# Performance work log

Measured on AMD Instinct MI355X. Metric: run time of the kernel, lower is better.

The kernel has to match this reference:

```python
import jax, jax.numpy as jnp
import numpy as np

B, L, D = 16, 2048, 256

def setup_inputs() -> dict:
    key = jax.random.key(0)
    k1, k2 = jax.random.split(key)
    inp = jax.random.normal(k1, (B, L, D), dtype=jnp.float32)
    # Linear(2*dim, 1, bias=False) weight, torch layout [out=1, in=2*dim]
    v_w = jax.random.normal(k2, (1, 2 * D), dtype=jnp.float32) * (1.0 / np.sqrt(2 * D))
    return {"inp": inp, "v_w": v_w}


def reference(inp, v_w):
    # score[b,i,j] = cat(query=inp[b,i], key=inp[b,j]) . v_w
    # decomposes exactly into two rank-1 projections broadcast-summed.
    dim = inp.shape[-1]
    wq = v_w[0, :dim]   # multiplies the query half (unsqueeze(1) -> index i)
    wk = v_w[0, dim:]   # multiplies the key half (unsqueeze(2) -> index j)
    sq = jnp.einsum('bld,d->bl', inp, wq)          # [B,L]
    sk = jnp.einsum('bld,d->bl', inp, wk)          # [B,L]
    score = sq[:, :, None] + sk[:, None, :]        # [B,L,L]
    attn = jax.nn.softmax(score, axis=2)           # Softmax(2)
    out = jnp.einsum('bij,bjd->bid', attn, inp)    # bmm
    return (out, attn)
```

## Files before the change

### kernel.cpp

```cpp
#include <hip/hip_runtime.h>

#define BB 16
#define LL 2048
#define DD 256
#define CH 32
#define NCH (LL / CH)

typedef float vf4 __attribute__((ext_vector_type(4)));

__global__ void k1_sk(const float* __restrict__ inp, const float* __restrict__ wk,
                      float* __restrict__ sk) {
    int tid  = threadIdx.x;
    int wid  = tid >> 6, lane = tid & 63;
    int row  = blockIdx.x * 4 + wid;
    const float4 a = *reinterpret_cast<const float4*>(inp + (size_t)row * DD + lane * 4);
    const float4 w = *reinterpret_cast<const float4*>(wk + lane * 4);
    float dot = a.x * w.x + a.y * w.y + a.z * w.z + a.w * w.w;
    #pragma unroll
    for (int off = 32; off >= 1; off >>= 1) dot += __shfl_down(dot, off, 64);
    if (lane == 0) sk[row] = dot;
}

__global__ void k2_softmax(const float* __restrict__ sk, float* __restrict__ p) {
    int b = blockIdx.x;
    int tid = threadIdx.x;
    int lane = tid & 63, wid = tid >> 6;
    const float* skb = sk + b * LL;
    float v[8];
    #pragma unroll
    for (int r = 0; r < 8; ++r) v[r] = skb[tid + r * 256];
    float mx = v[0];
    #pragma unroll
    for (int r = 1; r < 8; ++r) mx = fmaxf(mx, v[r]);
    __shared__ float sm[4];
    __shared__ float bc;
    #pragma unroll
    for (int off = 32; off >= 1; off >>= 1) mx = fmaxf(mx, __shfl_down(mx, off, 64));
    if (lane == 0) sm[wid] = mx;
    __syncthreads();
    if (tid == 0) bc = fmaxf(fmaxf(sm[0], sm[1]), fmaxf(sm[2], sm[3]));
    __syncthreads();
    float m = bc;
    float e[8], s = 0.f;
    #pragma unroll
    for (int r = 0; r < 8; ++r) { e[r] = __expf(v[r] - m); s += e[r]; }
    #pragma unroll
    for (int off = 32; off >= 1; off >>= 1) s += __shfl_down(s, off, 64);
    __syncthreads();
    if (lane == 0) sm[wid] = s;
    __syncthreads();
    if (tid == 0) bc = (sm[0] + sm[1]) + (sm[2] + sm[3]);
    __syncthreads();
    float inv = 1.0f / bc;
    #pragma unroll
    for (int r = 0; r < 8; ++r) p[b * LL + tid + r * 256] = e[r] * inv;
}

__global__ void k3a_partial(const float* __restrict__ inp, const float* __restrict__ p,
                            float* __restrict__ partial) {
    int blk = blockIdx.x;
    int b = blk >> 6, jc = blk & 63;
    int t = threadIdx.x;
    const float* pb = p + b * LL + jc * CH;
    const float* ib = inp + ((size_t)(b * LL + jc * CH)) * DD + t;
    float acc = 0.f;
    #pragma unroll 8
    for (int j = 0; j < CH; ++j) acc += pb[j] * ib[(size_t)j * DD];
    partial[(size_t)blk * DD + t] = acc;
}

__global__ void k3b_reduce(const float* __restrict__ partial, float* __restrict__ out_vec) {
    int b = blockIdx.x;
    int t = threadIdx.x;
    float acc = 0.f;
    #pragma unroll 8
    for (int jc = 0; jc < NCH; ++jc) acc += partial[((size_t)(b * NCH + jc)) * DD + t];
    out_vec[b * DD + t] = acc;
}

__global__ void k4_write(const vf4* __restrict__ outv4, const vf4* __restrict__ p4,
                         vf4* __restrict__ dst) {
    const size_t OUT4 = (size_t)BB * LL * DD / 4;
    const size_t TOT4 = OUT4 + (size_t)BB * LL * LL / 4;
    size_t stride = (size_t)gridDim.x * blockDim.x;
    for (size_t i = blockIdx.x * (size_t)blockDim.x + threadIdx.x; i < TOT4; i += stride) {
        vf4 v;
        if (i < OUT4) {
            size_t b  = i >> 17;
            size_t d4 = i & 63;
            v = outv4[(b << 6) + d4];
        } else {
            size_t k  = i - OUT4;
            size_t b  = k >> 20;
            size_t j4 = k & 511;
            v = p4[(b << 9) + j4];
        }
        __builtin_nontemporal_store(v, &dst[i]);
    }
}

extern "C" void kernel_launch(void* const* d_in, const int* in_sizes, int n_in,
                              void* d_out, int out_size, void* d_ws, size_t ws_size,
                              hipStream_t stream) {
    const float* inp = (const float*)d_in[0];
    const float* vw  = (const float*)d_in[1];
    float* out = (float*)d_out;
    float* ws  = (float*)d_ws;

    float* sk      = ws;
    float* p       = ws + 32768;
    float* partial = ws + 65536;
    float* out_vec = ws + 327680;

    k1_sk      <<<8192, 256, 0, stream>>>(inp, vw + DD, sk);
    k2_softmax <<<BB,   256, 0, stream>>>(sk, p);
    k3a_partial<<<BB * NCH, 256, 0, stream>>>(inp, p, partial);
    k3b_reduce <<<BB,   256, 0, stream>>>(partial, out_vec);
    k4_write   <<<2048, 256, 0, stream>>>((const vf4*)out_vec, (const vf4*)p,
                                          (vf4*)out);
}
```

Baseline: 78.92 us.

## Fuse key projection, exp and weighted sum into one pass without max subtraction

Result: faster. 72.46 us (-8.2%).

```diff
diff --git a/kernel.cpp b/kernel.cpp
--- a/kernel.cpp
+++ b/kernel.cpp
@@ -3,86 +3,82 @@
 #define BB 16
 #define LL 2048
 #define DD 256
-#define CH 32
-#define NCH (LL / CH)
 
 typedef float vf4 __attribute__((ext_vector_type(4)));
 
-__global__ void k1_sk(const float* __restrict__ inp, const float* __restrict__ wk,
-                      float* __restrict__ sk) {
-    int tid  = threadIdx.x;
-    int wid  = tid >> 6, lane = tid & 63;
-    int row  = blockIdx.x * 4 + wid;
-    const float4 a = *reinterpret_cast<const float4*>(inp + (size_t)row * DD + lane * 4);
+__global__ void __launch_bounds__(256)
+k1_pass(const float* __restrict__ inp, const float* __restrict__ wk,
+        float* __restrict__ e, float* __restrict__ upart, float* __restrict__ zpart) {
+    const int t = threadIdx.x, lane = t & 63, wid = t >> 6;
+    const int blk = blockIdx.x;
+    const int row0 = blk * 16 + wid * 4;
+
     const float4 w = *reinterpret_cast<const float4*>(wk + lane * 4);
-    float dot = a.x * w.x + a.y * w.y + a.z * w.z + a.w * w.w;
+    float4 acc = make_float4(0.f, 0.f, 0.f, 0.f);
+    float zsum = 0.f;
+
     #pragma unroll
-    for (int off = 32; off >= 1; off >>= 1) dot += __shfl_down(dot, off, 64);
-    if (lane == 0) sk[row] = dot;
+    for (int r = 0; r < 4; ++r) {
+        const int row = row0 + r;
+        const float4 a = *reinterpret_cast<const float4*>(inp + (size_t)row * DD + lane * 4);
+        float dot = a.x * w.x + a.y * w.y + a.z * w.z + a.w * w.w;
+        #pragma unroll
+        for (int off = 32; off >= 1; off >>= 1) dot += __shfl_xor(dot, off, 64);
+        const float ev = __expf(dot);
+        if (lane == 0) e[row] = ev;
+        zsum += ev;
+        acc.x = fmaf(ev, a.x, acc.x);
+        acc.y = fmaf(ev, a.y, acc.y);
+        acc.z = fmaf(ev, a.z, acc.z);
+        acc.w = fmaf(ev, a.w, acc.w);
+    }
+
+    __shared__ float uacc[4][DD];
+    __shared__ float zw[4];
+    *reinterpret_cast<float4*>(&uacc[wid][lane * 4]) = acc;
+    if (lane == 0) zw[wid] = zsum;
+    __syncthreads();
+    float u = uacc[0][t] + uacc[1][t] + uacc[2][t] + uacc[3][t];
+    upart[(size_t)blk * DD + t] = u;
+    if (t == 0) zpart[blk] = zw[0] + zw[1] + zw[2] + zw[3];
 }
 
-__global__ void k2_softmax(const float* __restrict__ sk, float* __restrict__ p) {
-    int b = blockIdx.x;
-    int tid = threadIdx.x;
-    int lane = tid & 63, wid = tid >> 6;
-    const float* skb = sk + b * LL;
-    float v[8];
+__global__ void __launch_bounds__(256)
+k2_finalize(const float* __restrict__ upart, const float* __restrict__ zpart,
+            const float* __restrict__ e, float* __restrict__ p,
+            float* __restrict__ out_vec) {
+    const int b = blockIdx.x, t = threadIdx.x;
+    __shared__ float zs[128];
+    __shared__ float Zsh;
+    if (t < 128) zs[t] = zpart[b * 128 + t];
+    __syncthreads();
+    if (t == 0) {
+        float z = 0.f;
+        #pragma unroll 8
+        for (int i = 0; i < 128; ++i) z += zs[i];
+        Zsh = z;
+    }
+    __syncthreads();
+    const float invZ = 1.0f / Zsh;
+
+    float acc = 0.f;
+    #pragma unroll 8
+    for (int c = 0; c < 128; ++c) acc += upart[((size_t)(b * 128 + c)) * DD + t];
+    out_vec[b * DD + t] = acc * invZ;
+
     #pragma unroll
-    for (int r = 0; r < 8; ++r) v[r] = skb[tid + r * 256];
-    float mx = v[0];
-    #pragma unroll
-    for (int r = 1; r < 8; ++r) mx = fmaxf(mx, v[r]);
-    __shared__ float sm[4];
-    __shared__ float bc;
-    #pragma unroll
-    for (int off = 32; off >= 1; off >>= 1) mx = fmaxf(mx, __shfl_down(mx, off, 64));
-    if (lane == 0) sm[wid] = mx;
-    __syncthreads();
-    if (tid == 0) bc = fmaxf(fmaxf(sm[0], sm[1]), fmaxf(sm[2], sm[3]));
-    __syncthreads();
-    float m = bc;
-    float e[8], s = 0.f;
-    #pragma unroll
-    for (int r = 0; r < 8; ++r) { e[r] = __expf(v[r] - m); s += e[r]; }
-    #pragma unroll
-    for (int off = 32; off >= 1; off >>= 1) s += __shfl_down(s, off, 64);
-    __syncthreads();
-    if (lane == 0) sm[wid] = s;
-    __syncthreads();
-    if (tid == 0) bc = (sm[0] + sm[1]) + (sm[2] + sm[3]);
-    __syncthreads();
-    float inv = 1.0f / bc;
-    #pragma unroll
-    for (int r = 0; r < 8; ++r) p[b * LL + tid + r * 256] = e[r] * inv;
+    for (int r = 0; r < 8; ++r) {
+        int j = r * 256 + t;
+        p[b * LL + j] = e[b * LL + j] * invZ;
+    }
 }
 
-__global__ void k3a_partial(const float* __restrict__ inp, const float* __restrict__ p,
-                            float* __restrict__ partial) {
-    int blk = blockIdx.x;
-    int b = blk >> 6, jc = blk & 63;
-    int t = threadIdx.x;
-    const float* pb = p + b * LL + jc * CH;
-    const float* ib = inp + ((size_t)(b * LL + jc * CH)) * DD + t;
-    float acc = 0.f;
-    #pragma unroll 8
-    for (int j = 0; j < CH; ++j) acc += pb[j] * ib[(size_t)j * DD];
-    partial[(size_t)blk * DD + t] = acc;
-}
-
-__global__ void k3b_reduce(const float* __restrict__ partial, float* __restrict__ out_vec) {
-    int b = blockIdx.x;
-    int t = threadIdx.x;
-    float acc = 0.f;
-    #pragma unroll 8
-    for (int jc = 0; jc < NCH; ++jc) acc += partial[((size_t)(b * NCH + jc)) * DD + t];
-    out_vec[b * DD + t] = acc;
-}
-
-__global__ void k4_write(const vf4* __restrict__ outv4, const vf4* __restrict__ p4,
-                         vf4* __restrict__ dst) {
+__global__ void __launch_bounds__(256)
+k3_write(const vf4* __restrict__ outv4, const vf4* __restrict__ p4,
+         vf4* __restrict__ dst) {
     const size_t OUT4 = (size_t)BB * LL * DD / 4;
     const size_t TOT4 = OUT4 + (size_t)BB * LL * LL / 4;
-    size_t stride = (size_t)gridDim.x * blockDim.x;
+    const size_t stride = (size_t)gridDim.x * blockDim.x;
     for (size_t i = blockIdx.x * (size_t)blockDim.x + threadIdx.x; i < TOT4; i += stride) {
         vf4 v;
         if (i < OUT4) {
@@ -107,15 +103,14 @@
     float* out = (float*)d_out;
     float* ws  = (float*)d_ws;
 
-    float* sk      = ws;
-    float* p       = ws + 32768;
-    float* partial = ws + 65536;
-    float* out_vec = ws + 327680;
+    float* e       = ws;
+    float* upart   = ws + 32768;
+    float* zpart   = ws + 557056;
+    float* p       = ws + 559104;
+    float* out_vec = ws + 591872;
 
-    k1_sk      <<<8192, 256, 0, stream>>>(inp, vw + DD, sk);
-    k2_softmax <<<BB,   256, 0, stream>>>(sk, p);
-    k3a_partial<<<BB * NCH, 256, 0, stream>>>(inp, p, partial);
-    k3b_reduce <<<BB,   256, 0, stream>>>(partial, out_vec);
-    k4_write   <<<2048, 256, 0, stream>>>((const vf4*)out_vec, (const vf4*)p,
+    k1_pass    <<<2048, 256, 0, stream>>>(inp, vw + DD, e, upart, zpart);
+    k2_finalize<<<BB,   256, 0, stream>>>(upart, zpart, e, p, out_vec);
+    k3_write   <<<2048, 256, 0, stream>>>((const vf4*)out_vec, (const vf4*)p,
                                           (vf4*)out);
 }
```
